# Performance work log

Hardware: AMD Instinct MI355X
Metric: run time of the kernel (lower is better)

The kernel has to match this reference:

```python
import jax, jax.numpy as jnp
import numpy as np

NUM_HEADS = 12


def setup_inputs() -> dict:
    key = jax.random.key(0)
    ks = jax.random.split(key, 5)
    B, N, C = 64, 388, 768  # N = 8*8*2 + 16*16 + 4
    return {
        "x": jax.random.normal(ks[0], (B, N, C), dtype=jnp.float32),
        "qkv_w": jax.random.normal(ks[1], (3 * C, C), dtype=jnp.float32) * 0.02,
        "qkv_b": jax.random.normal(ks[2], (3 * C,), dtype=jnp.float32) * 0.02,
        "proj_w": jax.random.normal(ks[3], (C, C), dtype=jnp.float32) * 0.02,
        "proj_b": jax.random.normal(ks[4], (C,), dtype=jnp.float32) * 0.02,
        "t_h": 8, "t_w": 8, "s_h": 16, "s_w": 16,
    }


def reference(x, qkv_w, qkv_b, proj_w, proj_b, t_h, t_w, s_h, s_w):
    B, N, C = x.shape
    H = NUM_HEADS
    D = C // H
    scale = D ** -0.5
    L_t = t_h * t_w * 2          # template (x2) tokens
    L_s = s_h * s_w + 4          # search tokens + 4 extra

    qkv = x @ qkv_w.T + qkv_b                       # [B,N,3C]
    qkv = qkv.reshape(B, N, 3, H, D).transpose(2, 0, 3, 1, 4)  # [3,B,H,N,D]
    q, k, v = qkv[0], qkv[1], qkv[2]                # each [B,H,N,D]

    q_mt, q_s = q[:, :, :L_t], q[:, :, L_t:]
    k_mt = k[:, :, :L_t]
    v_mt = v[:, :, :L_t]

    # template self-attention (template queries attend only to template keys)
    attn_mt = jax.nn.softmax(jnp.einsum("bhqd,bhkd->bhqk", q_mt, k_mt) * scale, axis=-1)
    x_mt = jnp.einsum("bhqk,bhkd->bhqd", attn_mt, v_mt)  # [B,H,L_t,D]
    x_mt = x_mt.transpose(0, 2, 1, 3).reshape(B, L_t, C)

    # search queries attend to ALL keys
    attn_s = jax.nn.softmax(jnp.einsum("bhqd,bhkd->bhqk", q_s, k) * scale, axis=-1)
    x_s = jnp.einsum("bhqk,bhkd->bhqd", attn_s, v)  # [B,H,L_s,D]
    x_s = x_s.transpose(0, 2, 1, 3).reshape(B, L_s, C)

    out = jnp.concatenate([x_mt, x_s], axis=1)      # [B,N,C]
    out = out @ proj_w.T + proj_b
    return out
```

## Files before the change

kernel.cpp:

```cpp
#include <hip/hip_runtime.h>
#include <cstdint>
#include <cstddef>
#include <cmath>

typedef __attribute__((ext_vector_type(4))) float f32x4;
typedef __attribute__((ext_vector_type(8))) short bf16x8;

typedef const __attribute__((address_space(1))) void* gas_ptr;
typedef __attribute__((address_space(3))) void* las_ptr;

static __device__ __forceinline__ short f2bf(float f) {
    union { float f; uint32_t u; } v; v.f = f;
    uint32_t r = v.u + 0x7fffu + ((v.u >> 16) & 1u);
    return (short)(r >> 16);
}

constexpr int MP = 25088;

__global__ void cvt_f32_bf16(const float* __restrict__ src, short* __restrict__ dst, int n4) {
    int i = blockIdx.x * blockDim.x + threadIdx.x;
    const int stride = gridDim.x * blockDim.x;
    for (; i < n4; i += stride) {
        const float4 v = reinterpret_cast<const float4*>(src)[i];
        short4 o;
        o.x = f2bf(v.x); o.y = f2bf(v.y); o.z = f2bf(v.z); o.w = f2bf(v.w);
        reinterpret_cast<short4*>(dst)[i] = o;
    }
}

__global__ void cvt_x_pad(const float* __restrict__ src, short* __restrict__ dst) {
    constexpr int N4 = MP * 768 / 4;
    int i = blockIdx.x * blockDim.x + threadIdx.x;
    const int stride = gridDim.x * blockDim.x;
    for (; i < N4; i += stride) {
        const int flat = i * 4;
        const int mp  = flat / 768;
        const int col = flat - mp * 768;
        const int b   = mp / 392;
        const int nn  = mp - b * 392;
        short4 o;
        if (nn < 388) {
            const float4 v = *reinterpret_cast<const float4*>(
                src + ((size_t)(b * 388 + nn) * 768 + col));
            o.x = f2bf(v.x); o.y = f2bf(v.y); o.z = f2bf(v.z); o.w = f2bf(v.w);
        } else {
            o.x = 0; o.y = 0; o.z = 0; o.w = 0;
        }
        reinterpret_cast<short4*>(dst)[i] = o;
    }
}

template<int MODE>
__global__ __launch_bounds__(256) void gemm_bt(
    const short* __restrict__ A, const short* __restrict__ Bw,
    const float* __restrict__ bias,
    short* __restrict__ qk, short* __restrict__ vT,
    float* __restrict__ fo, int NB)
{
    constexpr int K = 768;
    constexpr int KT = 12;
    __shared__ __align__(16) short ldsraw[2 * 128 * 64 * 2];
    short* ldsA = ldsraw;
    short* ldsB = ldsraw + 2 * 128 * 64;

    const int tid  = threadIdx.x;
    const int lane = tid & 63;
    const int wid  = tid >> 6;
    const int lrow = lane & 15;
    const int lgrp = lane >> 4;
    const int wr   = wid >> 1;
    const int wc   = wid & 1;

    const int nwg = gridDim.x;
    const int q8  = nwg >> 3, r8 = nwg & 7;
    const int xcd = blockIdx.x & 7, bidx = blockIdx.x >> 3;
    const int wgid = (xcd < r8 ? xcd * (q8 + 1) : r8 * (q8 + 1) + (xcd - r8) * q8) + bidx;
    const int m0 = (wgid / NB) * 128;
    const int n0 = (wgid % NB) * 128;

    f32x4 acc[4][4];
    #pragma unroll
    for (int i = 0; i < 4; ++i)
        #pragma unroll
        for (int j = 0; j < 4; ++j)
            acc[i][j] = f32x4{0.f, 0.f, 0.f, 0.f};

    auto stage = [&](int kt, int buf) {
        #pragma unroll
        for (int it = 0; it < 4; ++it) {
            const int c   = it * 256 + wid * 64 + lane;
            const int row = c >> 3;
            const int scb = ((c & 7) * 16) ^ ((row & 7) << 4);
            const short* ga = A  + (size_t)(m0 + row) * K + kt * 64 + (scb >> 1);
            const short* gb = Bw + (size_t)(n0 + row) * K + kt * 64 + (scb >> 1);
            __builtin_amdgcn_global_load_lds((gas_ptr)ga, (las_ptr)((char*)(ldsA + buf * 128 * 64) + c * 16), 16, 0, 0);
            __builtin_amdgcn_global_load_lds((gas_ptr)gb, (las_ptr)((char*)(ldsB + buf * 128 * 64) + c * 16), 16, 0, 0);
        }
    };

    stage(0, 0);

    for (int kt = 0; kt < KT; ++kt) {
        const int cur = kt & 1;
        if (kt + 1 < KT) {
            stage(kt + 1, cur ^ 1);
            asm volatile("s_waitcnt vmcnt(8)" ::: "memory");
        } else {
            asm volatile("s_waitcnt vmcnt(0)" ::: "memory");
        }
        __builtin_amdgcn_s_barrier();
        __builtin_amdgcn_sched_barrier(0);

        #pragma unroll
        for (int ks = 0; ks < 2; ++ks) {
            bf16x8 af[4], bfv[4];
            #pragma unroll
            for (int i = 0; i < 4; ++i) {
                const int r   = wr * 64 + i * 16 + lrow;
                const int byt = r * 128 + ((ks * 64 + lgrp * 16) ^ ((r & 7) << 4));
                af[i] = *reinterpret_cast<const bf16x8*>((const char*)(ldsA + cur * 128 * 64) + byt);
            }
            #pragma unroll
            for (int j = 0; j < 4; ++j) {
                const int r   = wc * 64 + j * 16 + lrow;
                const int byt = r * 128 + ((ks * 64 + lgrp * 16) ^ ((r & 7) << 4));
                bfv[j] = *reinterpret_cast<const bf16x8*>((const char*)(ldsB + cur * 128 * 64) + byt);
            }
            #pragma unroll
            for (int i = 0; i < 4; ++i)
                #pragma unroll
                for (int j = 0; j < 4; ++j)
                    acc[i][j] = __builtin_amdgcn_mfma_f32_16x16x32_bf16(af[i], bfv[j], acc[i][j], 0, 0, 0);
        }

        __builtin_amdgcn_sched_barrier(0);
        __builtin_amdgcn_s_barrier();
    }

    const int mb = m0 + wr * 64;
    const int nb = n0 + wc * 64;
    if constexpr (MODE == 0) {
        if (n0 < 1536) {
            #pragma unroll
            for (int j = 0; j < 4; ++j) {
                const int c  = nb + j * 16 + lrow;
                const float sc = (c < 768) ? 0.18033688011116f : 1.0f;
                const float bv = bias[c];
                #pragma unroll
                for (int i = 0; i < 4; ++i) {
                    #pragma unroll
                    for (int r = 0; r < 4; ++r) {
                        const int m = mb + i * 16 + lgrp * 4 + r;
                        qk[(size_t)m * 1536 + c] = f2bf((acc[i][j][r] + bv) * sc);
                    }
                }
            }
        } else {
            const int h = (nb - 1536) >> 6;
            short* lw = ldsraw + wid * (64 * 80);
            #pragma unroll
            for (int j = 0; j < 4; ++j) {
                const int dloc = j * 16 + lrow;
                const float bv = bias[nb + j * 16 + lrow];
                #pragma unroll
                for (int i = 0; i < 4; ++i)
                    #pragma unroll
                    for (int r = 0; r < 4; ++r)
                        lw[dloc * 80 + i * 16 + lgrp * 4 + r] = f2bf(acc[i][j][r] + bv);
            }
            asm volatile("s_waitcnt lgkmcnt(0)" ::: "memory");
            __builtin_amdgcn_sched_barrier(0);
            #pragma unroll
            for (int w = 0; w < 8; ++w) {
                const int d    = w * 8 + (lane >> 3);
                const int nloc = (lane & 7) * 8;
                const bf16x8 val = *reinterpret_cast<const bf16x8*>(lw + d * 80 + nloc);
                const int mchunk = mb + nloc;
                const int b  = mchunk / 392;
                const int nn = mchunk - b * 392;
                short* dst = vT + ((size_t)(b * 12 + h) * 64 + d) * 392 + nn;
                *reinterpret_cast<bf16x8*>(dst) = val;
            }
        }
    } else {
        #pragma unroll
        for (int i = 0; i < 4; ++i) {
            #pragma unroll
            for (int r = 0; r < 4; ++r) {
                const int m = mb + i * 16 + lgrp * 4 + r;
                #pragma unroll
                for (int j = 0; j < 4; ++j) {
                    const int c = nb + j * 16 + lrow;
                    fo[(size_t)m * 768 + c] = acc[i][j][r] + bias[c];
                }
            }
        }
    }
}

constexpr int PSTRB = 256;

template<int NT, bool VLDS>
static __device__ __forceinline__ void attn_chunk_lds(
    int kbeg, int k_len,
    const short* __restrict__ klds, const short* __restrict__ vlds,
    const short* __restrict__ vglob,
    const bf16x8 (&qf)[2], char* __restrict__ my,
    int lrow, int lgrp,
    float (&rs)[4], f32x4 (&oacc)[4])
{
    f32x4 sacc[NT];
    #pragma unroll
    for (int t = 0; t < NT; ++t) sacc[t] = f32x4{0.f, 0.f, 0.f, 0.f};

    #pragma unroll
    for (int t = 0; t < NT; ++t) {
        const int kl   = t * 16 + lrow;
        const int byt0 = kl * 128 + ((lgrp * 16) ^ ((kl & 7) << 4));
        const int byt1 = kl * 128 + ((64 + lgrp * 16) ^ ((kl & 7) << 4));
        const bf16x8 k0 = *reinterpret_cast<const bf16x8*>((const char*)klds + byt0);
        const bf16x8 k1 = *reinterpret_cast<const bf16x8*>((const char*)klds + byt1);
        sacc[t] = __builtin_amdgcn_mfma_f32_16x16x32_bf16(qf[0], k0, sacc[t], 0, 0, 0);
        sacc[t] = __builtin_amdgcn_mfma_f32_16x16x32_bf16(qf[1], k1, sacc[t], 0, 0, 0);
    }
    #pragma unroll
    for (int t = 0; t < NT; ++t) {
        const bool bad = (kbeg + t * 16 + lrow >= k_len);
        #pragma unroll
        for (int r = 0; r < 4; ++r) {
            const float p = bad ? 0.f : exp2f(sacc[t][r]);
            rs[r] += p;
            const int row = lgrp * 4 + r;
            const int byt = row * PSTRB + ((t * 32 + lrow * 2) ^ ((row & 7) << 4));
            *reinterpret_cast<short*>(my + byt) = f2bf(p);
        }
    }

    #pragma unroll
    for (int ks = 0; ks < NT / 2; ++ks) {
        const bf16x8 pf = *reinterpret_cast<const bf16x8*>(
            my + lrow * PSTRB + ((ks * 64 + lgrp * 16) ^ ((lrow & 7) << 4)));
        #pragma unroll
        for (int dt = 0; dt < 4; ++dt) {
            const int d = dt * 16 + lrow;
            const bf16x8 vf = VLDS
                ? *reinterpret_cast<const bf16x8*>((const char*)vlds + d * 256 + ((ks * 64 + lgrp * 16) ^ ((d & 7) << 4)))
                : *reinterpret_cast<const bf16x8*>(vglob + (size_t)d * 392 + ks * 32 + lgrp * 8);
            oacc[dt] = __builtin_amdgcn_mfma_f32_16x16x32_bf16(pf, vf, oacc[dt], 0, 0, 0);
        }
    }
}

__global__ __launch_bounds__(256, 4) void attn_flash(
    const short* __restrict__ qkb, const short* __restrict__ vT,
    short* __restrict__ ao)
{
    __shared__ __align__(16) short klds[128 * 64];
    __shared__ __align__(16) short vlds[64 * 128];
    __shared__ __align__(16) char  plds[4][16 * PSTRB];

    const int tid  = threadIdx.x;
    const int lane = tid & 63;
    const int wid  = tid >> 6;
    const int lrow = lane & 15;
    const int lgrp = lane >> 4;

    const int blk = blockIdx.x;
    const int xcd = blk & 7;
    const int i7  = blk >> 3;
    const int bh  = xcd * 96 + i7 / 7;
    const int bx  = i7 % 7;

    int q_start, qend, k_len, nfull;
    bool tail;
    if (bx < 2) { q_start = bx * 64;             qend = 128; k_len = 128; nfull = 1; tail = false; }
    else        { q_start = 128 + (bx - 2) * 64; qend = 388; k_len = 388; nfull = 3; tail = true;  }

    const int q0 = q_start + wid * 16;

    const int b = bh / 12, h = bh - b * 12;
    const short* qbase = qkb + (size_t)b * 392 * 1536 + h * 64;
    const short* kbase = qbase + 768;
    const short* vbase = vT + (size_t)bh * 64 * 392;

    int qrow = q0 + lrow; if (qrow >= qend) qrow = qend - 1;
    bf16x8 qf[2];
    #pragma unroll
    for (int ks = 0; ks < 2; ++ks)
        qf[ks] = *reinterpret_cast<const bf16x8*>(qbase + (size_t)qrow * 1536 + ks * 32 + lgrp * 8);

    float rs[4] = {0.f, 0.f, 0.f, 0.f};
    f32x4 oacc[4];
    #pragma unroll
    for (int dt = 0; dt < 4; ++dt) oacc[dt] = f32x4{0.f, 0.f, 0.f, 0.f};

    char* my = &plds[wid][0];

    for (int ch = 0; ch < nfull; ++ch) {
        const int kbeg = ch * 128;
        #pragma unroll
        for (int it = 0; it < 4; ++it) {
            const int c = it * 256 + tid;
            const int krow = c >> 3;
            const int kscb = ((c & 7) * 16) ^ ((krow & 7) << 4);
            const short* gk = kbase + (size_t)(kbeg + krow) * 1536 + (kscb >> 1);
            __builtin_amdgcn_global_load_lds((gas_ptr)gk, (las_ptr)((char*)klds + c * 16), 16, 0, 0);
            const int vrow = c >> 4;
            const int vscb = ((c & 15) * 16) ^ ((vrow & 7) << 4);
            const short* gv = vbase + (size_t)vrow * 392 + kbeg + (vscb >> 1);
            __builtin_amdgcn_global_load_lds((gas_ptr)gv, (las_ptr)((char*)vlds + c * 16), 16, 0, 0);
        }
        asm volatile("s_waitcnt vmcnt(0)" ::: "memory");
        __builtin_amdgcn_s_barrier();
        __builtin_amdgcn_sched_barrier(0);

        attn_chunk_lds<8, true>(kbeg, k_len, klds, vlds, nullptr, qf, my, lrow, lgrp, rs, oacc);

        __builtin_amdgcn_sched_barrier(0);
        __builtin_amdgcn_s_barrier();
    }

    if (tail) {
        {
            const int c = tid;
            const int krow = c >> 3;
            const int kscb = ((c & 7) * 16) ^ ((krow & 7) << 4);
            int g = 384 + krow; if (g > 391) g = 391;
            const short* gk = kbase + (size_t)g * 1536 + (kscb >> 1);
            __builtin_amdgcn_global_load_lds((gas_ptr)gk, (las_ptr)((char*)klds + c * 16), 16, 0, 0);
        }
        asm volatile("s_waitcnt vmcnt(0)" ::: "memory");
        __builtin_amdgcn_s_barrier();
        __builtin_amdgcn_sched_barrier(0);

        attn_chunk_lds<2, false>(384, k_len, klds, nullptr, vbase + 384, qf, my, lrow, lgrp, rs, oacc);
    }

    #pragma unroll
    for (int msk = 1; msk < 16; msk <<= 1)
        #pragma unroll
        for (int r = 0; r < 4; ++r) rs[r] += __shfl_xor(rs[r], msk, 64);

    float inv[4];
    #pragma unroll
    for (int r = 0; r < 4; ++r) inv[r] = 1.0f / rs[r];
    #pragma unroll
    for (int r = 0; r < 4; ++r) {
        const int qn = q0 + lgrp * 4 + r;
        if (qn < qend) {
            #pragma unroll
            for (int dt = 0; dt < 4; ++dt)
                ao[((size_t)b * 388 + qn) * 768 + h * 64 + dt * 16 + lrow] =
                    f2bf(oacc[dt][r] * inv[r]);
        }
    }
}

extern "C" void kernel_launch(void* const* d_in, const int* in_sizes, int n_in,
                              void* d_out, int out_size, void* d_ws, size_t ws_size,
                              hipStream_t stream) {
    (void)in_sizes; (void)n_in; (void)out_size; (void)ws_size;
    const float* x      = (const float*)d_in[0];
    const float* qkv_w  = (const float*)d_in[1];
    const float* qkv_b  = (const float*)d_in[2];
    const float* proj_w = (const float*)d_in[3];
    const float* proj_b = (const float*)d_in[4];
    float* out = (float*)d_out;

    char* ws = (char*)d_ws;
    short* xb   = (short*)(ws);
    short* attn = (short*)(ws);
    short* qkb  = (short*)(ws + 38535168);
    short* vTb  = (short*)(ws + 115605504);
    short* qwb  = (short*)(ws + 154140672);
    short* pwb  = (short*)(ws + 157679616);

    cvt_x_pad  <<<2048, 256, 0, stream>>>(x, xb);
    cvt_f32_bf16<<<512,  256, 0, stream>>>(qkv_w,  qwb, 2304 * 768 / 4);
    cvt_f32_bf16<<<256,  256, 0, stream>>>(proj_w, pwb, 768 * 768 / 4);

    gemm_bt<0><<<dim3(196 * 18), 256, 0, stream>>>(xb, qwb, qkv_b, qkb, vTb, nullptr, 18);

    attn_flash<<<dim3(5376), 256, 0, stream>>>(qkb, vTb, attn);

    gemm_bt<1><<<dim3(194 * 6), 256, 0, stream>>>(attn, pwb, proj_b, nullptr, nullptr, out, 6);
}
```

Before: 245.0 us.

## Double-buffer K/V LDS tiles in attention and group GEMM tile order

The attention kernel now double-buffers its K and V LDS tiles, issuing the next chunk's global-to-LDS loads before computing the current one and waiting with a partial vmcnt. Occupancy is lowered to 2 blocks per SM to fit the doubled LDS. Separately, the MODE 0 GEMM remaps workgroup ids into groups of 14 M-tiles per N column to improve L2 reuse. The aim is to hide load latency, at the cost of fewer resident blocks and a risky vmcnt count.

```diff
diff --git a/kernel.cpp b/kernel.cpp
--- a/kernel.cpp
+++ b/kernel.cpp
@@ -75,8 +75,20 @@
     const int q8  = nwg >> 3, r8 = nwg & 7;
     const int xcd = blockIdx.x & 7, bidx = blockIdx.x >> 3;
     const int wgid = (xcd < r8 ? xcd * (q8 + 1) : r8 * (q8 + 1) + (xcd - r8) * q8) + bidx;
-    const int m0 = (wgid / NB) * 128;
-    const int n0 = (wgid % NB) * 128;
+
+    int m0, n0;
+    if constexpr (MODE == 0) {
+        constexpr int G = 14, SG = G * 18;
+        const int mg = wgid / SG;
+        const int r  = wgid - mg * SG;
+        const int n  = r / G;
+        const int mi = r - n * G;
+        m0 = (mg * G + mi) * 128;
+        n0 = n * 128;
+    } else {
+        m0 = (wgid / NB) * 128;
+        n0 = (wgid % NB) * 128;
+    }
 
     f32x4 acc[4][4];
     #pragma unroll
@@ -251,12 +263,12 @@
     }
 }
 
-__global__ __launch_bounds__(256, 4) void attn_flash(
+__global__ __launch_bounds__(256, 2) void attn_flash(
     const short* __restrict__ qkb, const short* __restrict__ vT,
     short* __restrict__ ao)
 {
-    __shared__ __align__(16) short klds[128 * 64];
-    __shared__ __align__(16) short vlds[64 * 128];
+    __shared__ __align__(16) short klds[2][128 * 64];
+    __shared__ __align__(16) short vlds[2][64 * 128];
     __shared__ __align__(16) char  plds[4][16 * PSTRB];
 
     const int tid  = threadIdx.x;
@@ -296,7 +308,7 @@
 
     char* my = &plds[wid][0];
 
-    for (int ch = 0; ch < nfull; ++ch) {
+    auto stage_full = [&](int ch, int buf) {
         const int kbeg = ch * 128;
         #pragma unroll
         for (int it = 0; it < 4; ++it) {
@@ -304,17 +316,29 @@
             const int krow = c >> 3;
             const int kscb = ((c & 7) * 16) ^ ((krow & 7) << 4);
             const short* gk = kbase + (size_t)(kbeg + krow) * 1536 + (kscb >> 1);
-            __builtin_amdgcn_global_load_lds((gas_ptr)gk, (las_ptr)((char*)klds + c * 16), 16, 0, 0);
+            __builtin_amdgcn_global_load_lds((gas_ptr)gk, (las_ptr)((char*)&klds[buf][0] + c * 16), 16, 0, 0);
             const int vrow = c >> 4;
             const int vscb = ((c & 15) * 16) ^ ((vrow & 7) << 4);
             const short* gv = vbase + (size_t)vrow * 392 + kbeg + (vscb >> 1);
-            __builtin_amdgcn_global_load_lds((gas_ptr)gv, (las_ptr)((char*)vlds + c * 16), 16, 0, 0);
-        }
-        asm volatile("s_waitcnt vmcnt(0)" ::: "memory");
+            __builtin_amdgcn_global_load_lds((gas_ptr)gv, (las_ptr)((char*)&vlds[buf][0] + c * 16), 16, 0, 0);
+        }
+    };
+
+    stage_full(0, 0);
+
+    for (int ch = 0; ch < nfull; ++ch) {
+        const int cur = ch & 1;
+        if (ch + 1 < nfull) {
+            stage_full(ch + 1, cur ^ 1);
+            asm volatile("s_waitcnt vmcnt(8)" ::: "memory");
+        } else {
+            asm volatile("s_waitcnt vmcnt(0)" ::: "memory");
+        }
         __builtin_amdgcn_s_barrier();
         __builtin_amdgcn_sched_barrier(0);
 
-        attn_chunk_lds<8, true>(kbeg, k_len, klds, vlds, nullptr, qf, my, lrow, lgrp, rs, oacc);
+        attn_chunk_lds<8, true>(ch * 128, k_len, &klds[cur][0], &vlds[cur][0],
+                                nullptr, qf, my, lrow, lgrp, rs, oacc);
 
         __builtin_amdgcn_sched_barrier(0);
         __builtin_amdgcn_s_barrier();
@@ -327,13 +351,14 @@
             const int kscb = ((c & 7) * 16) ^ ((krow & 7) << 4);
             int g = 384 + krow; if (g > 391) g = 391;
             const short* gk = kbase + (size_t)g * 1536 + (kscb >> 1);
-            __builtin_amdgcn_global_load_lds((gas_ptr)gk, (las_ptr)((char*)klds + c * 16), 16, 0, 0);
+            __builtin_amdgcn_global_load_lds((gas_ptr)gk, (las_ptr)((char*)&klds[0][0] + c * 16), 16, 0, 0);
         }
         asm volatile("s_waitcnt vmcnt(0)" ::: "memory");
         __builtin_amdgcn_s_barrier();
         __builtin_amdgcn_sched_barrier(0);
 
-        attn_chunk_lds<2, false>(384, k_len, klds, nullptr, vbase + 384, qf, my, lrow, lgrp, rs, oacc);
+        attn_chunk_lds<2, false>(384, k_len, &klds[0][0], nullptr, vbase + 384,
+                                 qf, my, lrow, lgrp, rs, oacc);
     }
 
     #pragma unroll
```

Result: no change. 242.5 us (-1.0%).
